# Optimization experiments

Hardware: AMD Instinct MI355X
Metric: run time of the kernel (lower is better)

The kernel has to match this reference:

```python
import jax, jax.numpy as jnp
import numpy as np

N = 50000
E = 800000
D_IN = 128
D_HID = 256


def setup_inputs() -> dict:
    key = jax.random.key(0)
    ks = jax.random.split(key, 12)
    s = 0.02
    return {
        "node_features": jax.random.normal(ks[0], (N, D_IN), dtype=jnp.float32),
        "edge_index": jax.random.randint(ks[1], (2, E), 0, N, dtype=jnp.int64),
        # layer 0 (input_dim -> hidden)
        "eps0": jnp.zeros((), dtype=jnp.float32),
        "W1_0": jax.random.normal(ks[2], (D_IN, D_HID), dtype=jnp.float32) * s,
        "b1_0": jnp.zeros((D_HID,), dtype=jnp.float32),
        "W2_0": jax.random.normal(ks[3], (D_HID, D_HID), dtype=jnp.float32) * s,
        "b2_0": jnp.zeros((D_HID,), dtype=jnp.float32),
        # layer 1 (hidden -> hidden)
        "eps1": jnp.zeros((), dtype=jnp.float32),
        "W1_1": jax.random.normal(ks[4], (D_HID, D_HID), dtype=jnp.float32) * s,
        "b1_1": jnp.zeros((D_HID,), dtype=jnp.float32),
        "W2_1": jax.random.normal(ks[5], (D_HID, D_HID), dtype=jnp.float32) * s,
        "b2_1": jnp.zeros((D_HID,), dtype=jnp.float32),
        # fc_out (hidden -> input_dim)
        "Wo": jax.random.normal(ks[6], (D_HID, D_IN), dtype=jnp.float32) * s,
        "bo": jnp.zeros((D_IN,), dtype=jnp.float32),
    }


def _gin_layer(x, src, dst, eps, W1, b1, W2, b2):
    # gather neighbor features + scatter-add into destination nodes
    agg = jnp.zeros_like(x).at[dst].add(x[src])  # [N, d]
    h = (1.0 + eps) * x + agg
    h = jax.nn.relu(h @ W1 + b1)
    return h @ W2 + b2


def reference(node_features, edge_index, eps0, W1_0, b1_0, W2_0, b2_0,
              eps1, W1_1, b1_1, W2_1, b2_1, Wo, bo):
    src, dst = edge_index[0], edge_index[1]
    h = _gin_layer(node_features, src, dst, eps0, W1_0, b1_0, W2_0, b2_0)
    h = _gin_layer(h, src, dst, eps1, W1_1, b1_1, W2_1, b2_1)
    return h @ Wo + bo  # [N, input_dim]
```

## Files before the change

### kernel.cpp

```cpp
#include <hip/hip_runtime.h>

#define NN 50000
#define NE 800000
#define DIN 128
#define DHID 256
#define MAXDEG 128

typedef __bf16 bf16x8 __attribute__((ext_vector_type(8)));
typedef float f32x4 __attribute__((ext_vector_type(4)));

static __device__ __forceinline__ unsigned short f2bf(float f) {
    unsigned u = __float_as_uint(f);
    unsigned r = 0x7fffu + ((u >> 16) & 1u);
    return (unsigned short)((u + r) >> 16);
}
static __device__ __forceinline__ float blo(unsigned u) { return __uint_as_float(u << 16); }
static __device__ __forceinline__ float bhi(unsigned u) { return __uint_as_float(u & 0xffff0000u); }


__global__ void bucket_kernel(const int* __restrict__ src, const int* __restrict__ dst,
                              int* __restrict__ cnt, int* __restrict__ srcs, int E) {
    int i4 = (blockIdx.x * blockDim.x + threadIdx.x) * 4;
    if (i4 >= E) return;
    int4 d4 = *(const int4*)&dst[i4];
    int4 s4 = *(const int4*)&src[i4];
    int t0 = atomicAdd(&cnt[d4.x], 1);
    int t1 = atomicAdd(&cnt[d4.y], 1);
    int t2 = atomicAdd(&cnt[d4.z], 1);
    int t3 = atomicAdd(&cnt[d4.w], 1);
    if (t0 < MAXDEG) srcs[(size_t)d4.x * MAXDEG + t0] = s4.x;
    if (t1 < MAXDEG) srcs[(size_t)d4.y * MAXDEG + t1] = s4.y;
    if (t2 < MAXDEG) srcs[(size_t)d4.z * MAXDEG + t2] = s4.z;
    if (t3 < MAXDEG) srcs[(size_t)d4.w * MAXDEG + t3] = s4.w;
}


__global__ void convert_x_kernel(const float* __restrict__ x, unsigned short* __restrict__ xb,
                                 int* __restrict__ cnt, int n) {
    int i = blockIdx.x * blockDim.x + threadIdx.x;
    if (i < NN) cnt[i] = 0;
    if (i * 4 < n) {
        float4 v = *(const float4*)(x + (size_t)i * 4);
        ushort4 o;
        o.x = f2bf(v.x); o.y = f2bf(v.y); o.z = f2bf(v.z); o.w = f2bf(v.w);
        *(ushort4*)(xb + (size_t)i * 4) = o;
    }
}

__global__ void convert_w_kernel(const float* __restrict__ W1_0, const float* __restrict__ W2_0,
                                 const float* __restrict__ W1_1, const float* __restrict__ W2_1,
                                 const float* __restrict__ Wo,
                                 unsigned short* __restrict__ w10t, unsigned short* __restrict__ w20t,
                                 unsigned short* __restrict__ w11t, unsigned short* __restrict__ w21t,
                                 unsigned short* __restrict__ wot) {
    int i = blockIdx.x * blockDim.x + threadIdx.x;
    const float* W; unsigned short* Wt; int K, N, idx;
    if (i < 32768)        { W = W1_0; Wt = w10t; K = 128; N = 256; idx = i; }
    else if (i < 98304)   { W = W2_0; Wt = w20t; K = 256; N = 256; idx = i - 32768; }
    else if (i < 163840)  { W = W1_1; Wt = w11t; K = 256; N = 256; idx = i - 98304; }
    else if (i < 229376)  { W = W2_1; Wt = w21t; K = 256; N = 256; idx = i - 163840; }
    else if (i < 262144)  { W = Wo;   Wt = wot;  K = 256; N = 128; idx = i - 229376; }
    else return;
    int k = idx / N;
    int n = idx - k * N;
    Wt[(size_t)n * K + k] = f2bf(W[idx]);
}


template <int D>
__global__ void agg_bf16_kernel(const unsigned short* __restrict__ x, const int* __restrict__ cnt,
                                const int* __restrict__ srcs, const float* __restrict__ eps_p,
                                unsigned short* __restrict__ out, int n) {
    int gtid = blockIdx.x * blockDim.x + threadIdx.x;
    int node = gtid >> 6;
    int lane = threadIdx.x & 63;
    if (node >= n) return;
    int deg = cnt[node]; if (deg > MAXDEG) deg = MAXDEG;
    const int* sp = srcs + (size_t)node * MAXDEG;
    float e = 1.0f + eps_p[0];
    if constexpr (D == 128) {
        const unsigned* xp = (const unsigned*)x;
        float a0 = 0.f, a1 = 0.f, b0 = 0.f, b1 = 0.f;
        int i = 0;
        for (; i + 4 <= deg; i += 4) {
            int sA = sp[i], sB = sp[i + 1], sC = sp[i + 2], sD = sp[i + 3];
            unsigned vA = xp[(size_t)sA * 64 + lane];
            unsigned vB = xp[(size_t)sB * 64 + lane];
            unsigned vC = xp[(size_t)sC * 64 + lane];
            unsigned vD = xp[(size_t)sD * 64 + lane];
            a0 += blo(vA); a1 += bhi(vA);
            b0 += blo(vB); b1 += bhi(vB);
            a0 += blo(vC); a1 += bhi(vC);
            b0 += blo(vD); b1 += bhi(vD);
        }
        for (; i < deg; i++) {
            unsigned v = xp[(size_t)sp[i] * 64 + lane];
            a0 += blo(v); a1 += bhi(v);
        }
        unsigned xv = xp[(size_t)node * 64 + lane];
        a0 += b0 + e * blo(xv);
        a1 += b1 + e * bhi(xv);
        ((unsigned*)out)[(size_t)node * 64 + lane] =
            (unsigned)f2bf(a0) | ((unsigned)f2bf(a1) << 16);
    } else {
        const uint2* xp = (const uint2*)x;
        float a0 = 0.f, a1 = 0.f, a2 = 0.f, a3 = 0.f;
        float b0 = 0.f, b1 = 0.f, b2 = 0.f, b3 = 0.f;
        int i = 0;
        for (; i + 4 <= deg; i += 4) {
            int sA = sp[i], sB = sp[i + 1], sC = sp[i + 2], sD = sp[i + 3];
            uint2 vA = xp[(size_t)sA * 64 + lane];
            uint2 vB = xp[(size_t)sB * 64 + lane];
            uint2 vC = xp[(size_t)sC * 64 + lane];
            uint2 vD = xp[(size_t)sD * 64 + lane];
            a0 += blo(vA.x); a1 += bhi(vA.x); a2 += blo(vA.y); a3 += bhi(vA.y);
            b0 += blo(vB.x); b1 += bhi(vB.x); b2 += blo(vB.y); b3 += bhi(vB.y);
            a0 += blo(vC.x); a1 += bhi(vC.x); a2 += blo(vC.y); a3 += bhi(vC.y);
            b0 += blo(vD.x); b1 += bhi(vD.x); b2 += blo(vD.y); b3 += bhi(vD.y);
        }
        for (; i < deg; i++) {
            uint2 v = xp[(size_t)sp[i] * 64 + lane];
            a0 += blo(v.x); a1 += bhi(v.x); a2 += blo(v.y); a3 += bhi(v.y);
        }
        uint2 xv = xp[(size_t)node * 64 + lane];
        a0 += b0 + e * blo(xv.x);
        a1 += b1 + e * bhi(xv.x);
        a2 += b2 + e * blo(xv.y);
        a3 += b3 + e * bhi(xv.y);
        uint2 o;
        o.x = (unsigned)f2bf(a0) | ((unsigned)f2bf(a1) << 16);
        o.y = (unsigned)f2bf(a2) | ((unsigned)f2bf(a3) << 16);
        ((uint2*)out)[(size_t)node * 64 + lane] = o;
    }
}


template <int K, int NWN, int MT, int F32OUT, int RELU>
__global__ __launch_bounds__(256, 2) void gemm_direct(
        const unsigned short* __restrict__ A, const unsigned short* __restrict__ Wt,
        const float* __restrict__ bias, unsigned short* __restrict__ Cb,
        float* __restrict__ Cf, int M, int T, int G) {
    constexpr int N = NWN * 64;
    constexpr int MW = 4 / NWN;
    constexpr int MTILE = MW * MT * 16;
    constexpr int NKS = K / 32;

    const int tid = threadIdx.x;
    const int lane = tid & 63;
    const int w = tid >> 6;
    const int quad = lane >> 4;
    const int l16 = lane & 15;
    const int nsl = w % NWN;
    const int msub = w / NWN;

    bf16x8 bfrag[NKS][4];
    #pragma unroll
    for (int ks = 0; ks < NKS; ks++)
        #pragma unroll
        for (int nt = 0; nt < 4; nt++)
            bfrag[ks][nt] = *(const bf16x8*)&Wt[(size_t)(nsl * 64 + nt * 16 + l16) * K + ks * 32 + quad * 8];

    f32x4 bvv[4];
    #pragma unroll
    for (int nt = 0; nt < 4; nt++)
        bvv[nt] = *(const f32x4*)&bias[nsl * 64 + nt * 16 + quad * 4];

    for (int t = blockIdx.x; t < T; t += G) {
        size_t rowbase = (size_t)t * MTILE;
        bf16x8 af[MT][NKS];
        #pragma unroll
        for (int j = 0; j < MT; j++) {
            const unsigned short* ar =
                A + (rowbase + (size_t)(msub * MT + j) * 16 + l16) * K + quad * 8;
            #pragma unroll
            for (int ks = 0; ks < NKS; ks++) af[j][ks] = *(const bf16x8*)(ar + ks * 32);
        }
        #pragma unroll
        for (int j = 0; j < MT; j++) {
            f32x4 acc[4];
            #pragma unroll
            for (int nt = 0; nt < 4; nt++) acc[nt] = (f32x4)(0.f);
            #pragma unroll
            for (int ks = 0; ks < NKS; ks++)
                #pragma unroll
                for (int nt = 0; nt < 4; nt++)
                    acc[nt] = __builtin_amdgcn_mfma_f32_16x16x32_bf16(bfrag[ks][nt], af[j][ks], acc[nt], 0, 0, 0);
            size_t gm = rowbase + (size_t)(msub * MT + j) * 16 + l16;
            if (gm < (size_t)M) {
                #pragma unroll
                for (int nt = 0; nt < 4; nt++) {
                    f32x4 v = acc[nt] + bvv[nt];
                    if (RELU) {
                        v[0] = fmaxf(v[0], 0.f); v[1] = fmaxf(v[1], 0.f);
                        v[2] = fmaxf(v[2], 0.f); v[3] = fmaxf(v[3], 0.f);
                    }
                    int gn = nsl * 64 + nt * 16 + quad * 4;
                    if (F32OUT) {
                        *(f32x4*)&Cf[gm * N + gn] = v;
                    } else {
                        uint2 o;
                        o.x = (unsigned)f2bf(v[0]) | ((unsigned)f2bf(v[1]) << 16);
                        o.y = (unsigned)f2bf(v[2]) | ((unsigned)f2bf(v[3]) << 16);
                        *(uint2*)&Cb[gm * N + gn] = o;
                    }
                }
            }
        }
    }
}


static inline size_t align256(size_t v) { return (v + 255) & ~(size_t)255; }

extern "C" void kernel_launch(void* const* d_in, const int* in_sizes, int n_in,
                              void* d_out, int out_size, void* d_ws, size_t ws_size,
                              hipStream_t stream) {
    const float* x        = (const float*)d_in[0];
    const int*   ei       = (const int*)d_in[1];
    const float* eps0     = (const float*)d_in[2];
    const float* W1_0     = (const float*)d_in[3];
    const float* b1_0     = (const float*)d_in[4];
    const float* W2_0     = (const float*)d_in[5];
    const float* b2_0     = (const float*)d_in[6];
    const float* eps1     = (const float*)d_in[7];
    const float* W1_1     = (const float*)d_in[8];
    const float* b1_1     = (const float*)d_in[9];
    const float* W2_1     = (const float*)d_in[10];
    const float* b2_1     = (const float*)d_in[11];
    const float* Wo       = (const float*)d_in[12];
    const float* bo       = (const float*)d_in[13];
    float* out            = (float*)d_out;

    const int* srcE = ei;
    const int* dstE = ei + NE;

    char* p = (char*)d_ws;
    size_t o = 0;
    int* cnt  = (int*)(p + o); o = align256(o + (size_t)NN * 4);
    int* srcs = (int*)(p + o); o = align256(o + (size_t)NN * MAXDEG * 4);
    unsigned short* xb   = (unsigned short*)(p + o); o = align256(o + (size_t)NN * DIN * 2);
    unsigned short* w10t = (unsigned short*)(p + o); o = align256(o + (size_t)DHID * DIN * 2);
    unsigned short* w20t = (unsigned short*)(p + o); o = align256(o + (size_t)DHID * DHID * 2);
    unsigned short* w11t = (unsigned short*)(p + o); o = align256(o + (size_t)DHID * DHID * 2);
    unsigned short* w21t = (unsigned short*)(p + o); o = align256(o + (size_t)DHID * DHID * 2);
    unsigned short* wot  = (unsigned short*)(p + o); o = align256(o + (size_t)DIN * DHID * 2);
    unsigned short* bufA = (unsigned short*)(p + o); o = align256(o + (size_t)NN * DHID * 2 + 65536);
    unsigned short* bufB = (unsigned short*)(p + o); o = align256(o + (size_t)NN * DHID * 2 + 65536);

    convert_x_kernel<<<(NN * DIN / 4 + 255) / 256, 256, 0, stream>>>(x, xb, cnt, NN * DIN);
    bucket_kernel<<<(NE / 4 + 255) / 256, 256, 0, stream>>>(srcE, dstE, cnt, srcs, NE);
    convert_w_kernel<<<(262144 + 255) / 256, 256, 0, stream>>>(
        W1_0, W2_0, W1_1, W2_1, Wo, w10t, w20t, w11t, w21t, wot);

    int aggBlocks = (NN * 64 + 255) / 256;
    const int G = 512;
    const int T32 = (NN + 31) / 32;
    const int T64 = (NN + 63) / 64;

    agg_bf16_kernel<DIN><<<aggBlocks, 256, 0, stream>>>(xb, cnt, srcs, eps0, bufA, NN);
    gemm_direct<128, 4, 2, 0, 1><<<G, 256, 0, stream>>>(bufA, w10t, b1_0, bufB, nullptr, NN, T32, G);
    gemm_direct<256, 4, 2, 0, 0><<<G, 256, 0, stream>>>(bufB, w20t, b2_0, bufA, nullptr, NN, T32, G);

    agg_bf16_kernel<DHID><<<aggBlocks, 256, 0, stream>>>(bufA, cnt, srcs, eps1, bufB, NN);
    gemm_direct<256, 4, 2, 0, 1><<<G, 256, 0, stream>>>(bufB, w11t, b1_1, bufA, nullptr, NN, T32, G);
    gemm_direct<256, 4, 2, 0, 0><<<G, 256, 0, stream>>>(bufA, w21t, b2_1, bufB, nullptr, NN, T32, G);

    gemm_direct<256, 2, 2, 1, 0><<<G, 256, 0, stream>>>(bufB, wot, bo, nullptr, out, NN, T64, G);
}
```

Baseline: 359.5 us.

## Fuse per-layer MLP GEMMs through LDS and merge prep kernels

Replaces the separate per-layer GEMM launches with a fused MLP kernel. Each block handles 64 rows and keeps the hidden activations in swizzled shared memory, so layer 0 runs two GEMMs per launch and layer 1 plus the output projection run three. This removes global round-trips of the intermediate activations and several launches. The weight and input conversion kernels are merged into one prep kernel, and the aggregation loop now issues eight gathers per iteration instead of four. In exchange, each block reloads all weight fragments per 64-row tile instead of persisting across tiles, and uses more LDS, which may lower occupancy.

```diff
diff --git a/kernel.cpp b/kernel.cpp
--- a/kernel.cpp
+++ b/kernel.cpp
@@ -35,35 +35,33 @@
 }
 
 
-__global__ void convert_x_kernel(const float* __restrict__ x, unsigned short* __restrict__ xb,
-                                 int* __restrict__ cnt, int n) {
+__global__ void prep_kernel(const float* __restrict__ x, unsigned short* __restrict__ xb,
+                            int* __restrict__ cnt,
+                            const float* __restrict__ W1_0, const float* __restrict__ W2_0,
+                            const float* __restrict__ W1_1, const float* __restrict__ W2_1,
+                            const float* __restrict__ Wo,
+                            unsigned short* __restrict__ w10t, unsigned short* __restrict__ w20t,
+                            unsigned short* __restrict__ w11t, unsigned short* __restrict__ w21t,
+                            unsigned short* __restrict__ wot) {
     int i = blockIdx.x * blockDim.x + threadIdx.x;
     if (i < NN) cnt[i] = 0;
-    if (i * 4 < n) {
+    if (i < 262144) {
+        const float* W; unsigned short* Wt; int K, N, idx;
+        if (i < 32768)        { W = W1_0; Wt = w10t; K = 128; N = 256; idx = i; }
+        else if (i < 98304)   { W = W2_0; Wt = w20t; K = 256; N = 256; idx = i - 32768; }
+        else if (i < 163840)  { W = W1_1; Wt = w11t; K = 256; N = 256; idx = i - 98304; }
+        else if (i < 229376)  { W = W2_1; Wt = w21t; K = 256; N = 256; idx = i - 163840; }
+        else                  { W = Wo;   Wt = wot;  K = 256; N = 128; idx = i - 229376; }
+        int k = idx / N;
+        int n = idx - k * N;
+        Wt[(size_t)n * K + k] = f2bf(W[idx]);
+    }
+    if (i * 4 < NN * DIN) {
         float4 v = *(const float4*)(x + (size_t)i * 4);
         ushort4 o;
         o.x = f2bf(v.x); o.y = f2bf(v.y); o.z = f2bf(v.z); o.w = f2bf(v.w);
         *(ushort4*)(xb + (size_t)i * 4) = o;
     }
-}
-
-__global__ void convert_w_kernel(const float* __restrict__ W1_0, const float* __restrict__ W2_0,
-                                 const float* __restrict__ W1_1, const float* __restrict__ W2_1,
-                                 const float* __restrict__ Wo,
-                                 unsigned short* __restrict__ w10t, unsigned short* __restrict__ w20t,
-                                 unsigned short* __restrict__ w11t, unsigned short* __restrict__ w21t,
-                                 unsigned short* __restrict__ wot) {
-    int i = blockIdx.x * blockDim.x + threadIdx.x;
-    const float* W; unsigned short* Wt; int K, N, idx;
-    if (i < 32768)        { W = W1_0; Wt = w10t; K = 128; N = 256; idx = i; }
-    else if (i < 98304)   { W = W2_0; Wt = w20t; K = 256; N = 256; idx = i - 32768; }
-    else if (i < 163840)  { W = W1_1; Wt = w11t; K = 256; N = 256; idx = i - 98304; }
-    else if (i < 229376)  { W = W2_1; Wt = w21t; K = 256; N = 256; idx = i - 163840; }
-    else if (i < 262144)  { W = Wo;   Wt = wot;  K = 256; N = 128; idx = i - 229376; }
-    else return;
-    int k = idx / N;
-    int n = idx - k * N;
-    Wt[(size_t)n * K + k] = f2bf(W[idx]);
 }
 
 
@@ -82,16 +80,15 @@
         const unsigned* xp = (const unsigned*)x;
         float a0 = 0.f, a1 = 0.f, b0 = 0.f, b1 = 0.f;
         int i = 0;
-        for (; i + 4 <= deg; i += 4) {
-            int sA = sp[i], sB = sp[i + 1], sC = sp[i + 2], sD = sp[i + 3];
-            unsigned vA = xp[(size_t)sA * 64 + lane];
-            unsigned vB = xp[(size_t)sB * 64 + lane];
-            unsigned vC = xp[(size_t)sC * 64 + lane];
-            unsigned vD = xp[(size_t)sD * 64 + lane];
-            a0 += blo(vA); a1 += bhi(vA);
-            b0 += blo(vB); b1 += bhi(vB);
-            a0 += blo(vC); a1 += bhi(vC);
-            b0 += blo(vD); b1 += bhi(vD);
+        for (; i + 8 <= deg; i += 8) {
+            unsigned v[8];
+            #pragma unroll
+            for (int j = 0; j < 8; j++) v[j] = xp[(size_t)sp[i + j] * 64 + lane];
+            #pragma unroll
+            for (int j = 0; j < 8; j += 2) {
+                a0 += blo(v[j]);     a1 += bhi(v[j]);
+                b0 += blo(v[j + 1]); b1 += bhi(v[j + 1]);
+            }
         }
         for (; i < deg; i++) {
             unsigned v = xp[(size_t)sp[i] * 64 + lane];
@@ -107,16 +104,15 @@
         float a0 = 0.f, a1 = 0.f, a2 = 0.f, a3 = 0.f;
         float b0 = 0.f, b1 = 0.f, b2 = 0.f, b3 = 0.f;
         int i = 0;
-        for (; i + 4 <= deg; i += 4) {
-            int sA = sp[i], sB = sp[i + 1], sC = sp[i + 2], sD = sp[i + 3];
-            uint2 vA = xp[(size_t)sA * 64 + lane];
-            uint2 vB = xp[(size_t)sB * 64 + lane];
-            uint2 vC = xp[(size_t)sC * 64 + lane];
-            uint2 vD = xp[(size_t)sD * 64 + lane];
-            a0 += blo(vA.x); a1 += bhi(vA.x); a2 += blo(vA.y); a3 += bhi(vA.y);
-            b0 += blo(vB.x); b1 += bhi(vB.x); b2 += blo(vB.y); b3 += bhi(vB.y);
-            a0 += blo(vC.x); a1 += bhi(vC.x); a2 += blo(vC.y); a3 += bhi(vC.y);
-            b0 += blo(vD.x); b1 += bhi(vD.x); b2 += blo(vD.y); b3 += bhi(vD.y);
+        for (; i + 8 <= deg; i += 8) {
+            uint2 v[8];
+            #pragma unroll
+            for (int j = 0; j < 8; j++) v[j] = xp[(size_t)sp[i + j] * 64 + lane];
+            #pragma unroll
+            for (int j = 0; j < 8; j += 2) {
+                a0 += blo(v[j].x);     a1 += bhi(v[j].x);     a2 += blo(v[j].y);     a3 += bhi(v[j].y);
+                b0 += blo(v[j + 1].x); b1 += bhi(v[j + 1].x); b2 += blo(v[j + 1].y); b3 += bhi(v[j + 1].y);
+            }
         }
         for (; i < deg; i++) {
             uint2 v = xp[(size_t)sp[i] * 64 + lane];
@@ -135,74 +131,154 @@
 }
 
 
-template <int K, int NWN, int MT, int F32OUT, int RELU>
-__global__ __launch_bounds__(256, 2) void gemm_direct(
-        const unsigned short* __restrict__ A, const unsigned short* __restrict__ Wt,
-        const float* __restrict__ bias, unsigned short* __restrict__ Cb,
-        float* __restrict__ Cf, int M, int T, int G) {
-    constexpr int N = NWN * 64;
-    constexpr int MW = 4 / NWN;
-    constexpr int MTILE = MW * MT * 16;
-    constexpr int NKS = K / 32;
+template <int K1, int THREE>
+__global__ __launch_bounds__(256, 2) void mlp_fused(
+        const unsigned short* __restrict__ A,
+        const unsigned short* __restrict__ W1t, const float* __restrict__ b1,
+        const unsigned short* __restrict__ W2t, const float* __restrict__ b2,
+        const unsigned short* __restrict__ W3t, const float* __restrict__ b3,
+        unsigned short* __restrict__ Cb, float* __restrict__ Cf, int M) {
+    constexpr int NKS1 = K1 / 32;
+    __shared__ __align__(16) unsigned short H[(THREE ? 2 : 1) * 64 * 256];
+    unsigned short* H1 = H;
+    unsigned short* H2 = H + 64 * 256;
 
     const int tid = threadIdx.x;
     const int lane = tid & 63;
     const int w = tid >> 6;
     const int quad = lane >> 4;
     const int l16 = lane & 15;
-    const int nsl = w % NWN;
-    const int msub = w / NWN;
-
-    bf16x8 bfrag[NKS][4];
-    #pragma unroll
-    for (int ks = 0; ks < NKS; ks++)
+    const size_t rowbase = (size_t)blockIdx.x * 64;
+
+    bf16x8 bfrag[8][4];
+    f32x4 bvv[4];
+
+    #pragma unroll
+    for (int ks = 0; ks < NKS1; ks++)
         #pragma unroll
         for (int nt = 0; nt < 4; nt++)
-            bfrag[ks][nt] = *(const bf16x8*)&Wt[(size_t)(nsl * 64 + nt * 16 + l16) * K + ks * 32 + quad * 8];
-
-    f32x4 bvv[4];
+            bfrag[ks][nt] = *(const bf16x8*)&W1t[(size_t)(w * 64 + nt * 16 + l16) * K1 + ks * 32 + quad * 8];
     #pragma unroll
     for (int nt = 0; nt < 4; nt++)
-        bvv[nt] = *(const f32x4*)&bias[nsl * 64 + nt * 16 + quad * 4];
-
-    for (int t = blockIdx.x; t < T; t += G) {
-        size_t rowbase = (size_t)t * MTILE;
-        bf16x8 af[MT][NKS];
-        #pragma unroll
-        for (int j = 0; j < MT; j++) {
-            const unsigned short* ar =
-                A + (rowbase + (size_t)(msub * MT + j) * 16 + l16) * K + quad * 8;
-            #pragma unroll
-            for (int ks = 0; ks < NKS; ks++) af[j][ks] = *(const bf16x8*)(ar + ks * 32);
-        }
-        #pragma unroll
-        for (int j = 0; j < MT; j++) {
-            f32x4 acc[4];
-            #pragma unroll
-            for (int nt = 0; nt < 4; nt++) acc[nt] = (f32x4)(0.f);
-            #pragma unroll
-            for (int ks = 0; ks < NKS; ks++)
-                #pragma unroll
-                for (int nt = 0; nt < 4; nt++)
-                    acc[nt] = __builtin_amdgcn_mfma_f32_16x16x32_bf16(bfrag[ks][nt], af[j][ks], acc[nt], 0, 0, 0);
-            size_t gm = rowbase + (size_t)(msub * MT + j) * 16 + l16;
+        bvv[nt] = *(const f32x4*)&b1[w * 64 + nt * 16 + quad * 4];
+
+    #pragma unroll
+    for (int j = 0; j < 4; j++) {
+        const unsigned short* ar = A + (rowbase + j * 16 + l16) * K1 + quad * 8;
+        bf16x8 af[NKS1];
+        #pragma unroll
+        for (int ks = 0; ks < NKS1; ks++) af[ks] = *(const bf16x8*)(ar + ks * 32);
+        f32x4 acc[4];
+        #pragma unroll
+        for (int nt = 0; nt < 4; nt++) acc[nt] = (f32x4)(0.f);
+        #pragma unroll
+        for (int ks = 0; ks < NKS1; ks++)
+            #pragma unroll
+            for (int nt = 0; nt < 4; nt++)
+                acc[nt] = __builtin_amdgcn_mfma_f32_16x16x32_bf16(bfrag[ks][nt], af[ks], acc[nt], 0, 0, 0);
+        int r = j * 16 + l16;
+        #pragma unroll
+        for (int nt = 0; nt < 4; nt++) {
+            f32x4 v = acc[nt] + bvv[nt];
+            v[0] = fmaxf(v[0], 0.f); v[1] = fmaxf(v[1], 0.f);
+            v[2] = fmaxf(v[2], 0.f); v[3] = fmaxf(v[3], 0.f);
+            int c = w * 8 + nt * 2 + (quad >> 1);
+            int cs = c ^ (r & 7);
+            uint2 o;
+            o.x = (unsigned)f2bf(v[0]) | ((unsigned)f2bf(v[1]) << 16);
+            o.y = (unsigned)f2bf(v[2]) | ((unsigned)f2bf(v[3]) << 16);
+            *(uint2*)&H1[r * 256 + cs * 8 + (quad & 1) * 4] = o;
+        }
+    }
+    __syncthreads();
+
+    #pragma unroll
+    for (int ks = 0; ks < 8; ks++)
+        #pragma unroll
+        for (int nt = 0; nt < 4; nt++)
+            bfrag[ks][nt] = *(const bf16x8*)&W2t[(size_t)(w * 64 + nt * 16 + l16) * 256 + ks * 32 + quad * 8];
+    #pragma unroll
+    for (int nt = 0; nt < 4; nt++)
+        bvv[nt] = *(const f32x4*)&b2[w * 64 + nt * 16 + quad * 4];
+
+    #pragma unroll
+    for (int j = 0; j < 4; j++) {
+        int r = j * 16 + l16;
+        bf16x8 af[8];
+        #pragma unroll
+        for (int ks = 0; ks < 8; ks++) {
+            int cs = (ks * 4 + quad) ^ (r & 7);
+            af[ks] = *(const bf16x8*)&H1[r * 256 + cs * 8];
+        }
+        f32x4 acc[4];
+        #pragma unroll
+        for (int nt = 0; nt < 4; nt++) acc[nt] = (f32x4)(0.f);
+        #pragma unroll
+        for (int ks = 0; ks < 8; ks++)
+            #pragma unroll
+            for (int nt = 0; nt < 4; nt++)
+                acc[nt] = __builtin_amdgcn_mfma_f32_16x16x32_bf16(bfrag[ks][nt], af[ks], acc[nt], 0, 0, 0);
+        if constexpr (!THREE) {
+            size_t gm = rowbase + j * 16 + l16;
             if (gm < (size_t)M) {
                 #pragma unroll
                 for (int nt = 0; nt < 4; nt++) {
                     f32x4 v = acc[nt] + bvv[nt];
-                    if (RELU) {
-                        v[0] = fmaxf(v[0], 0.f); v[1] = fmaxf(v[1], 0.f);
-                        v[2] = fmaxf(v[2], 0.f); v[3] = fmaxf(v[3], 0.f);
-                    }
-                    int gn = nsl * 64 + nt * 16 + quad * 4;
-                    if (F32OUT) {
-                        *(f32x4*)&Cf[gm * N + gn] = v;
-                    } else {
-                        uint2 o;
-                        o.x = (unsigned)f2bf(v[0]) | ((unsigned)f2bf(v[1]) << 16);
-                        o.y = (unsigned)f2bf(v[2]) | ((unsigned)f2bf(v[3]) << 16);
-                        *(uint2*)&Cb[gm * N + gn] = o;
-                    }
+                    uint2 o;
+                    o.x = (unsigned)f2bf(v[0]) | ((unsigned)f2bf(v[1]) << 16);
+                    o.y = (unsigned)f2bf(v[2]) | ((unsigned)f2bf(v[3]) << 16);
+                    *(uint2*)&Cb[gm * 256 + w * 64 + nt * 16 + quad * 4] = o;
+                }
+            }
+        } else {
+            #pragma unroll
+            for (int nt = 0; nt < 4; nt++) {
+                f32x4 v = acc[nt] + bvv[nt];
+                int c = w * 8 + nt * 2 + (quad >> 1);
+                int cs = c ^ (r & 7);
+                uint2 o;
+                o.x = (unsigned)f2bf(v[0]) | ((unsigned)f2bf(v[1]) << 16);
+                o.y = (unsigned)f2bf(v[2]) | ((unsigned)f2bf(v[3]) << 16);
+                *(uint2*)&H2[r * 256 + cs * 8 + (quad & 1) * 4] = o;
+            }
+        }
+    }
+
+    if constexpr (THREE) {
+        __syncthreads();
+        #pragma unroll
+        for (int ks = 0; ks < 8; ks++)
+            #pragma unroll
+            for (int nt = 0; nt < 2; nt++)
+                bfrag[ks][nt] = *(const bf16x8*)&W3t[(size_t)(w * 32 + nt * 16 + l16) * 256 + ks * 32 + quad * 8];
+        f32x4 bv3[2];
+        #pragma unroll
+        for (int nt = 0; nt < 2; nt++)
+            bv3[nt] = *(const f32x4*)&b3[w * 32 + nt * 16 + quad * 4];
+
+        #pragma unroll
+        for (int j = 0; j < 4; j++) {
+            int r = j * 16 + l16;
+            bf16x8 af[8];
+            #pragma unroll
+            for (int ks = 0; ks < 8; ks++) {
+                int cs = (ks * 4 + quad) ^ (r & 7);
+                af[ks] = *(const bf16x8*)&H2[r * 256 + cs * 8];
+            }
+            f32x4 acc[2];
+            #pragma unroll
+            for (int nt = 0; nt < 2; nt++) acc[nt] = (f32x4)(0.f);
+            #pragma unroll
+            for (int ks = 0; ks < 8; ks++)
+                #pragma unroll
+                for (int nt = 0; nt < 2; nt++)
+                    acc[nt] = __builtin_amdgcn_mfma_f32_16x16x32_bf16(bfrag[ks][nt], af[ks], acc[nt], 0, 0, 0);
+            size_t gm = rowbase + j * 16 + l16;
+            if (gm < (size_t)M) {
+                #pragma unroll
+                for (int nt = 0; nt < 2; nt++) {
+                    f32x4 v = acc[nt] + bv3[nt];
+                    *(f32x4*)&Cf[gm * 128 + w * 32 + nt * 16 + quad * 4] = v;
                 }
             }
         }
@@ -247,23 +323,18 @@
     unsigned short* bufA = (unsigned short*)(p + o); o = align256(o + (size_t)NN * DHID * 2 + 65536);
     unsigned short* bufB = (unsigned short*)(p + o); o = align256(o + (size_t)NN * DHID * 2 + 65536);
 
-    convert_x_kernel<<<(NN * DIN / 4 + 255) / 256, 256, 0, stream>>>(x, xb, cnt, NN * DIN);
+    prep_kernel<<<(NN * DIN / 4 + 255) / 256, 256, 0, stream>>>(
+        x, xb, cnt, W1_0, W2_0, W1_1, W2_1, Wo, w10t, w20t, w11t, w21t, wot);
     bucket_kernel<<<(NE / 4 + 255) / 256, 256, 0, stream>>>(srcE, dstE, cnt, srcs, NE);
-    convert_w_kernel<<<(262144 + 255) / 256, 256, 0, stream>>>(
-        W1_0, W2_0, W1_1, W2_1, Wo, w10t, w20t, w11t, w21t, wot);
 
     int aggBlocks = (NN * 64 + 255) / 256;
-    const int G = 512;
-    const int T32 = (NN + 31) / 32;
-    const int T64 = (NN + 63) / 64;
+    int mlpBlocks = (NN + 63) / 64;
 
     agg_bf16_kernel<DIN><<<aggBlocks, 256, 0, stream>>>(xb, cnt, srcs, eps0, bufA, NN);
-    gemm_direct<128, 4, 2, 0, 1><<<G, 256, 0, stream>>>(bufA, w10t, b1_0, bufB, nullptr, NN, T32, G);
-    gemm_direct<256, 4, 2, 0, 0><<<G, 256, 0, stream>>>(bufB, w20t, b2_0, bufA, nullptr, NN, T32, G);
-
-    agg_bf16_kernel<DHID><<<aggBlocks, 256, 0, stream>>>(bufA, cnt, srcs, eps1, bufB, NN);
-    gemm_direct<256, 4, 2, 0, 1><<<G, 256, 0, stream>>>(bufB, w11t, b1_1, bufA, nullptr, NN, T32, G);
-    gemm_direct<256, 4, 2, 0, 0><<<G, 256, 0, stream>>>(bufA, w21t, b2_1, bufB, nullptr, NN, T32, G);
-
-    gemm_direct<256, 2, 2, 1, 0><<<G, 256, 0, stream>>>(bufB, wot, bo, nullptr, out, NN, T64, G);
-}
+    mlp_fused<128, 0><<<mlpBlocks, 256, 0, stream>>>(
+        bufA, w10t, b1_0, w20t, b2_0, nullptr, nullptr, bufB, nullptr, NN);
+
+    agg_bf16_kernel<DHID><<<aggBlocks, 256, 0, stream>>>(bufB, cnt, srcs, eps1, bufA, NN);
+    mlp_fused<256, 1><<<mlpBlocks, 256, 0, stream>>>(
+        bufA, w11t, b1_1, w21t, b2_1, wot, bo, nullptr, out, NN);
+}
```

After: 348.2 us. 3.2% less time.
